# Optimization experiments

Measured on AMD Instinct MI355X. Metric: run time of the kernel, lower is better.

Reference implementation:

```python
import jax, jax.numpy as jnp
import numpy as np

DIM = 512
N_HEADS = 8
N_KV_HEADS = 4
HEAD_DIM = DIM // N_HEADS  # 64
N_REP = N_HEADS // N_KV_HEADS  # 2
THETA = 10000.0
EPS_RMS = 1e-6
EPS_Z = 1e-6


def setup_inputs() -> dict:
    key = jax.random.key(0)
    ks = jax.random.split(key, 6)
    s = 1.0 / np.sqrt(DIM)
    return {
        "x": jax.random.normal(ks[0], (4, 8192, DIM), dtype=jnp.float32),
        "norm_w": jnp.ones((DIM,), dtype=jnp.float32),
        "wq": jax.random.normal(ks[1], (DIM, DIM), dtype=jnp.float32) * s,
        "wk": jax.random.normal(ks[2], (N_KV_HEADS * HEAD_DIM, DIM), dtype=jnp.float32) * s,
        "wv": jax.random.normal(ks[3], (N_KV_HEADS * HEAD_DIM, DIM), dtype=jnp.float32) * s,
        "wo": jax.random.normal(ks[4], (DIM, DIM), dtype=jnp.float32) * s,
    }


def _rope_cos_sin(seq_len, head_dim):
    # freqs_cis = polar(1, t * theta^(-2i/d))
    inv = 1.0 / (THETA ** (jnp.arange(0, head_dim, 2, dtype=jnp.float32) / head_dim))
    ang = jnp.arange(seq_len, dtype=jnp.float32)[:, None] * inv[None, :]  # (S, d/2)
    return jnp.cos(ang), jnp.sin(ang)


def _apply_rope(t, cos, sin):
    # t: (B, S, H, d); complex rotation on consecutive pairs
    B, S, H, d = t.shape
    tr = t.reshape(B, S, H, d // 2, 2)
    xr, xi = tr[..., 0], tr[..., 1]
    c = cos[None, :, None, :]  # (1, S, 1, d/2)
    s = sin[None, :, None, :]
    out = jnp.stack([xr * c - xi * s, xr * s + xi * c], axis=-1)
    return out.reshape(B, S, H, d)


def _forward(x, norm_w, wq, wk, wv, wo):
    B, S, _ = x.shape
    # RMSNorm
    x = x * jax.lax.rsqrt(jnp.mean(x * x, axis=-1, keepdims=True) + EPS_RMS) * norm_w
    xq = (x @ wq.T).reshape(B, S, N_HEADS, HEAD_DIM)
    xk = (x @ wk.T).reshape(B, S, N_KV_HEADS, HEAD_DIM)
    xv = (x @ wv.T).reshape(B, S, N_KV_HEADS, HEAD_DIM)
    cos, sin = _rope_cos_sin(S, HEAD_DIM)
    xq = _apply_rope(xq, cos, sin)
    xk = _apply_rope(xk, cos, sin)
    # repeat_kv: (B,S,Hkv,d) -> (B,S,Hkv*n_rep,d)
    keys = jnp.repeat(xk, N_REP, axis=2)
    values = jnp.repeat(xv, N_REP, axis=2)
    # to (B, H, S, d)
    Q = jnp.transpose(xq, (0, 2, 1, 3))
    K = jnp.transpose(keys, (0, 2, 1, 3))
    V = jnp.transpose(values, (0, 2, 1, 3))
    phi = lambda t: jax.nn.elu(t) + 1.0
    Q_lin, K_lin = phi(Q), phi(K)
    # Faithful to source: elementwise product reduced over s -> (B,H,d)
    KV = jnp.einsum('bhsd,bhsd->bhd', K_lin, V)
    K_sum = K_lin.sum(axis=2)  # (B,H,d)
    Z = jnp.einsum('bhsd,bhd->bhs', Q_lin, K_sum)[..., None]  # (B,H,S,1)
    Y = Q_lin * KV[:, :, None, :] / (Z + EPS_Z)  # (B,H,S,d)
    Y = jnp.transpose(Y, (0, 2, 1, 3)).reshape(B, S, N_HEADS * HEAD_DIM)
    return Y @ wo.T


def reference(x, norm_w, wq, wk, wv, wo):
    return _forward(x, norm_w, wq, wk, wv, wo)
```

## Files before the change

### kernel.cpp

```cpp
#include <hip/hip_runtime.h>
#include <cmath>

typedef __attribute__((ext_vector_type(8))) short short8;
typedef __attribute__((ext_vector_type(4))) float floatx4;

#define T_TOK 32768
#define DIMK 512

__device__ __forceinline__ unsigned short f2bf(float f) {
  union { float f; unsigned int u; } v; v.f = f;
  unsigned int r = (v.u + 0x7fffu + ((v.u >> 16) & 1u)) >> 16;
  return (unsigned short)r;
}
__device__ __forceinline__ float bf2f(unsigned short h) {
  union { unsigned int u; float f; } v; v.u = ((unsigned int)h) << 16;
  return v.f;
}

__device__ __forceinline__ void gload_lds16(const unsigned short* g, unsigned short* ldsbase) {
  __builtin_amdgcn_global_load_lds(
      (const __attribute__((address_space(1))) unsigned int*)g,
      (__attribute__((address_space(3))) unsigned int*)ldsbase, 16, 0, 0);
}

__global__ __launch_bounds__(256) void k_prep(const float* __restrict__ x,
    const float* __restrict__ norm_w, const float* __restrict__ wq,
    const float* __restrict__ wk, const float* __restrict__ wv,
    const float* __restrict__ wo, unsigned short* __restrict__ Wb,
    unsigned short* __restrict__ wob, float2* __restrict__ rope,
    float* __restrict__ KVz, unsigned short* __restrict__ xn) {
  if (blockIdx.x < 2048) {
    int i = blockIdx.x * 256 + threadIdx.x;
    float v;
    if (i < 262144) {
      v = wq[i];
    } else {
      int R = i >> 9, col = i & 511;
      int h = (R - 512) >> 7, rem = (R - 512) & 127;
      if (rem < 64) v = wk[(h * 64 + rem) * 512 + col];
      else          v = wv[(h * 64 + rem - 64) * 512 + col];
    }
    Wb[i] = f2bf(v);
    if (i < 262144) {
      wob[i] = f2bf(wo[i]);
      int s = i >> 5, m = i & 31;
      const double c0 = 0.74989420933245582;
      double c1 = c0 * c0, c2 = c1 * c1, c3 = c2 * c2, c4 = c3 * c3;
      double p = 1.0;
      if (m & 1)  p *= c0;
      if (m & 2)  p *= c1;
      if (m & 4)  p *= c2;
      if (m & 8)  p *= c3;
      if (m & 16) p *= c4;
      double ang = (double)s * p;
      const double TWO_PI = 6.2831853071795864769;
      double q = rint(ang * (1.0 / TWO_PI));
      double r = fma(-q, TWO_PI, ang);
      float rf = (float)r;
      rope[i] = make_float2(cosf(rf), sinf(rf));
    }
    if (i < 2048) KVz[i] = 0.f;
  } else {
    int bid = blockIdx.x - 2048;
    int wave = threadIdx.x >> 6, lane = threadIdx.x & 63;
    size_t t = (size_t)bid * 4 + wave;
    const float4* xr = (const float4*)(x + t * DIMK);
    float4 a = xr[lane * 2];
    float4 b = xr[lane * 2 + 1];
    float ss = a.x * a.x + a.y * a.y + a.z * a.z + a.w * a.w
             + b.x * b.x + b.y * b.y + b.z * b.z + b.w * b.w;
    #pragma unroll
    for (int off = 32; off >= 1; off >>= 1) ss += __shfl_xor(ss, off, 64);
    float scale = rsqrtf(ss * (1.0f / DIMK) + 1e-6f);
    const float4* wr = (const float4*)norm_w;
    float4 w0 = wr[lane * 2], w1 = wr[lane * 2 + 1];
    uint4 o;
    o.x = (unsigned int)f2bf(a.x * scale * w0.x) | ((unsigned int)f2bf(a.y * scale * w0.y) << 16);
    o.y = (unsigned int)f2bf(a.z * scale * w0.z) | ((unsigned int)f2bf(a.w * scale * w0.w) << 16);
    o.z = (unsigned int)f2bf(b.x * scale * w1.x) | ((unsigned int)f2bf(b.y * scale * w1.y) << 16);
    o.w = (unsigned int)f2bf(b.z * scale * w1.z) | ((unsigned int)f2bf(b.w * scale * w1.w) << 16);
    *(uint4*)(xn + t * DIMK + lane * 8) = o;
  }
}

template <bool BF16_OUT, bool FUSE>
__global__ __launch_bounds__(512, 2) void k_gemm256(const unsigned short* __restrict__ A,
    const unsigned short* __restrict__ Bw, void* __restrict__ Cv, int ldc,
    const float2* __restrict__ rope, float* __restrict__ KV, float* __restrict__ Ksum) {
  constexpr int K = DIMK;
  extern __shared__ __align__(16) unsigned short smem[];
  unsigned short* const AsP = smem;
  unsigned short* const BsP = smem + 32768;

  const int tid = threadIdx.x;
  const int wave = tid >> 6, lane = tid & 63;
  const int r = lane & 15, quad = lane >> 4, r7 = r & 7;
  const int wm = (wave >> 2) * 128, wn = (wave & 3) * 64;

  const int ngy = gridDim.y;
  const int bid = blockIdx.x + gridDim.x * blockIdx.y;
  const int xcd = bid & 7;
  const int j = bid >> 3;
  const int lg = (ngy == 4) ? 2 : 1;
  const int per = (gridDim.x * ngy) >> (3 + lg);
  const int mt = xcd * per + (j >> lg);
  const int nt = j & (ngy - 1);
  const int m0 = mt * 256, n0 = nt * 256;

  const int srow = lane >> 3;
  const int scb = (lane & 7) ^ srow;
  const unsigned short* const Asrc = A + (size_t)(m0 + wave * 8 + srow) * K + scb * 8;
  const unsigned short* const Bsrc = Bw + (size_t)(n0 + wave * 8 + srow) * K + scb * 8;
  unsigned short* const Adst = AsP + wave * 8 * 64;
  unsigned short* const Bdst = BsP + wave * 8 * 64;

#define STAGE_A(buf, h, kt) do { \
    gload_lds16(Asrc + (size_t)((h) * 128) * K + (kt) * 64, Adst + (buf) * 16384 + ((h) * 128) * 64); \
    gload_lds16(Asrc + (size_t)((h) * 128 + 64) * K + (kt) * 64, Adst + (buf) * 16384 + ((h) * 128 + 64) * 64); \
  } while (0)
#define STAGE_B(buf, h, kt) do { \
    gload_lds16(Bsrc + (size_t)((h) * 128) * K + (kt) * 64, Bdst + (buf) * 16384 + ((h) * 128) * 64); \
    gload_lds16(Bsrc + (size_t)((h) * 128 + 64) * K + (kt) * 64, Bdst + (buf) * 16384 + ((h) * 128 + 64) * 64); \
  } while (0)

  short8 af[4][2], b0[2][2], b1[2][2];
  floatx4 acc[8][4];
  #pragma unroll
  for (int i = 0; i < 8; i++)
    #pragma unroll
    for (int jj = 0; jj < 4; jj++)
      acc[i][jj] = (floatx4){0.f, 0.f, 0.f, 0.f};

#define LDA8(buf, ah) do { \
    _Pragma("unroll") for (int ii = 0; ii < 4; ii++) \
      _Pragma("unroll") for (int kk = 0; kk < 2; kk++) \
        af[ii][kk] = *(const short8*)&AsP[(buf) * 16384 + (wm + (ah) * 64 + ii * 16 + r) * 64 + ((kk * 4 + quad) ^ r7) * 8]; \
  } while (0)
#define LDB4(buf, bh, arr) do { \
    _Pragma("unroll") for (int jj = 0; jj < 2; jj++) \
      _Pragma("unroll") for (int kk = 0; kk < 2; kk++) \
        arr[jj][kk] = *(const short8*)&BsP[(buf) * 16384 + (wn + (bh) * 32 + jj * 16 + r) * 64 + ((kk * 4 + quad) ^ r7) * 8]; \
  } while (0)
#define MFMAQ(ah, bh, arr) do { \
    __builtin_amdgcn_s_setprio(1); \
    _Pragma("unroll") for (int ii = 0; ii < 4; ii++) \
      _Pragma("unroll") for (int jj = 0; jj < 2; jj++) \
        _Pragma("unroll") for (int kk = 0; kk < 2; kk++) \
          acc[(ah) * 4 + ii][(bh) * 2 + jj] = __builtin_amdgcn_mfma_f32_16x16x32_bf16( \
              af[ii][kk], arr[jj][kk], acc[(ah) * 4 + ii][(bh) * 2 + jj], 0, 0, 0); \
    __builtin_amdgcn_s_setprio(0); \
  } while (0)
#define BAR() do { asm volatile("" ::: "memory"); __builtin_amdgcn_s_barrier(); asm volatile("" ::: "memory"); } while (0)
#define VMW(n) do { asm volatile("s_waitcnt vmcnt(" #n ")" ::: "memory"); __builtin_amdgcn_sched_barrier(0); } while (0)

  STAGE_A(0, 0, 0); STAGE_B(0, 0, 0); STAGE_A(0, 1, 0); STAGE_B(0, 1, 0);
  STAGE_A(1, 0, 1); STAGE_B(1, 0, 1); STAGE_A(1, 1, 1); STAGE_B(1, 1, 1);
  VMW(8);
  BAR();

  #pragma unroll
  for (int it = 0; it < 3; ++it) {
    const int kt = it * 2;
    LDA8(0, 0); LDB4(0, 0, b0);
    BAR(); MFMAQ(0, 0, b0); BAR();
    LDB4(0, 1, b1);
    BAR(); MFMAQ(0, 1, b1); BAR();
    LDA8(0, 1); STAGE_B(0, 0, kt + 2); STAGE_B(0, 1, kt + 2);
    BAR(); MFMAQ(1, 1, b1); BAR();
    STAGE_A(0, 0, kt + 2); STAGE_A(0, 1, kt + 2);
    BAR(); MFMAQ(1, 0, b0); VMW(8); BAR();
    LDA8(1, 0); LDB4(1, 0, b0);
    BAR(); MFMAQ(0, 0, b0); BAR();
    LDB4(1, 1, b1);
    BAR(); MFMAQ(0, 1, b1); BAR();
    LDA8(1, 1); STAGE_B(1, 0, kt + 3); STAGE_B(1, 1, kt + 3);
    BAR(); MFMAQ(1, 1, b1); BAR();
    STAGE_A(1, 0, kt + 3); STAGE_A(1, 1, kt + 3);
    BAR(); MFMAQ(1, 0, b0); VMW(8); BAR();
  }

  LDA8(0, 0); LDB4(0, 0, b0);
  BAR(); MFMAQ(0, 0, b0); BAR();
  LDB4(0, 1, b1);
  BAR(); MFMAQ(0, 1, b1); BAR();
  LDA8(0, 1);
  BAR(); MFMAQ(1, 1, b1); BAR();
  MFMAQ(1, 0, b0); VMW(0); BAR();
  LDA8(1, 0); LDB4(1, 0, b0);
  BAR(); MFMAQ(0, 0, b0); BAR();
  LDB4(1, 1, b1);
  BAR(); MFMAQ(0, 1, b1); BAR();
  LDA8(1, 1);
  BAR(); MFMAQ(1, 1, b1); BAR();
  MFMAQ(1, 0, b0);

  if (FUSE && n0 >= 512) {
    const int b = m0 >> 13;
    const int kh = ((n0 - 512) >> 8) * 2 + (wn >> 7);
    const int hvb = (wn >> 7) << 6;
    float* const Vs = (float*)smem;
    __syncthreads();
    if (wn & 64) {
      #pragma unroll
      for (int i = 0; i < 8; i++)
        #pragma unroll
        for (int j2 = 0; j2 < 4; j2++)
          #pragma unroll
          for (int p = 0; p < 4; p++) {
            int t = wm + i * 16 + quad * 4 + p;
            Vs[t * 128 + hvb + j2 * 16 + r] = acc[i][j2][p];
          }
    }
    __syncthreads();
    if (!(wn & 64)) {
      float kvp[4] = {0.f, 0.f, 0.f, 0.f};
      float ksp[4] = {0.f, 0.f, 0.f, 0.f};
      #pragma unroll
      for (int i = 0; i < 8; i++)
        #pragma unroll
        for (int p = 0; p < 4; p++) {
          int t = wm + i * 16 + quad * 4 + p;
          int pos = (m0 + t) & 8191;
          #pragma unroll
          for (int j2 = 0; j2 < 4; j2++) {
            float v = acc[i][j2][p];
            float vp = __shfl_xor(v, 1, 64);
            int d = j2 * 16 + r;
            float2 cs = rope[pos * 32 + (d >> 1)];
            float rk = (r & 1) ? (vp * cs.y + v * cs.x) : (v * cs.x - vp * cs.y);
            rk = rk > 0.f ? rk + 1.f : __expf(rk);
            kvp[j2] += rk * Vs[t * 128 + hvb + d];
            ksp[j2] += rk;
          }
        }
      #pragma unroll
      for (int j2 = 0; j2 < 4; j2++) {
        kvp[j2] += __shfl_xor(kvp[j2], 16, 64); kvp[j2] += __shfl_xor(kvp[j2], 32, 64);
        ksp[j2] += __shfl_xor(ksp[j2], 16, 64); ksp[j2] += __shfl_xor(ksp[j2], 32, 64);
      }
      if (lane < 16) {
        int base = (b * 4 + kh) * 64 + r;
        #pragma unroll
        for (int j2 = 0; j2 < 4; j2++) {
          atomicAdd(&KV[base + j2 * 16], kvp[j2]);
          atomicAdd(&Ksum[base + j2 * 16], ksp[j2]);
        }
      }
    }
  } else {
    #pragma unroll
    for (int i = 0; i < 8; i++)
      #pragma unroll
      for (int j2 = 0; j2 < 4; j2++) {
        int row = m0 + wm + i * 16 + quad * 4;
        int col = n0 + wn + j2 * 16 + r;
        #pragma unroll
        for (int p = 0; p < 4; p++) {
          if constexpr (BF16_OUT) {
            ((unsigned short*)Cv)[(size_t)(row + p) * ldc + col] = f2bf(acc[i][j2][p]);
          } else {
            ((float*)Cv)[(size_t)(row + p) * ldc + col] = acc[i][j2][p];
          }
        }
      }
  }
#undef STAGE_A
#undef STAGE_B
#undef LDA8
#undef LDB4
#undef MFMAQ
#undef BAR
#undef VMW
}

__global__ __launch_bounds__(256) void k_qkern(const unsigned short* __restrict__ qkv,
    const float2* __restrict__ rope, const float* __restrict__ KV,
    const float* __restrict__ Ksum, unsigned short* __restrict__ Yb) {
  const int h = threadIdx.x >> 5;
  const int pr = threadIdx.x & 31;
  for (int t = blockIdx.x; t < T_TOK; t += gridDim.x) {
    int b = t >> 13, pos = t & 8191;
    unsigned int qp = *(const unsigned int*)(qkv + (size_t)t * 512 + h * 64 + 2 * pr);
    float qx = bf2f((unsigned short)(qp & 0xffffu));
    float qy = bf2f((unsigned short)(qp >> 16));
    float2 cs = rope[pos * 32 + pr];
    float ar = qx * cs.x - qy * cs.y;
    float ai = qx * cs.y + qy * cs.x;
    ar = ar > 0.f ? ar + 1.f : __expf(ar);
    ai = ai > 0.f ? ai + 1.f : __expf(ai);
    int bk = b * 4 + (h >> 1);
    float2 ks = *(const float2*)(Ksum + bk * 64 + 2 * pr);
    float z = ar * ks.x + ai * ks.y;
    #pragma unroll
    for (int off = 16; off >= 1; off >>= 1) z += __shfl_xor(z, off, 64);
    float2 kv = *(const float2*)(KV + bk * 64 + 2 * pr);
    float inv = 1.0f / (z + 1e-6f);
    unsigned int o = (unsigned int)f2bf(ar * kv.x * inv)
                   | ((unsigned int)f2bf(ai * kv.y * inv) << 16);
    *(unsigned int*)(Yb + (size_t)t * 512 + h * 64 + 2 * pr) = o;
  }
}

extern "C" void kernel_launch(void* const* d_in, const int* in_sizes, int n_in,
                              void* d_out, int out_size, void* d_ws, size_t ws_size,
                              hipStream_t stream) {
  const float* x = (const float*)d_in[0];
  const float* norm_w = (const float*)d_in[1];
  const float* wq = (const float*)d_in[2];
  const float* wk = (const float*)d_in[3];
  const float* wv = (const float*)d_in[4];
  const float* wo = (const float*)d_in[5];
  float* out = (float*)d_out;

  char* ws = (char*)d_ws;
  unsigned short* xn  = (unsigned short*)(ws);
  unsigned short* Wb  = (unsigned short*)(ws + 33554432);
  unsigned short* wob = (unsigned short*)(ws + 34603008);
  unsigned short* qkv = (unsigned short*)(ws + 35127296);
  float2* rope        = (float2*)(ws + 102236160);
  float* KV           = (float*)(ws + 104333312);
  float* Ksum         = (float*)(ws + 104337408);
  unsigned short* Yb  = (unsigned short*)(ws + 104341504);

  static bool s_attr = false;
  if (!s_attr) {
    (void)hipFuncSetAttribute(reinterpret_cast<const void*>(&k_gemm256<true, true>),
                              hipFuncAttributeMaxDynamicSharedMemorySize, 131072);
    (void)hipFuncSetAttribute(reinterpret_cast<const void*>(&k_gemm256<false, false>),
                              hipFuncAttributeMaxDynamicSharedMemorySize, 131072);
    s_attr = true;
  }

  k_prep<<<10240, 256, 0, stream>>>(x, norm_w, wq, wk, wv, wo, Wb, wob, rope, KV, xn);
  k_gemm256<true, true><<<dim3(128, 4), 512, 131072, stream>>>(
      xn, Wb, (void*)qkv, 512, rope, KV, Ksum);
  k_qkern<<<4096, 256, 0, stream>>>(qkv, rope, KV, Ksum, Yb);
  k_gemm256<false, false><<<dim3(128, 2), 512, 131072, stream>>>(
      Yb, wob, (void*)out, 512, nullptr, nullptr, nullptr);
}
```

Baseline: 220.3 us.

## Store GEMM operands in K-panel-major layout and swizzle the V staging buffer

```diff
diff --git a/kernel.cpp b/kernel.cpp
--- a/kernel.cpp
+++ b/kernel.cpp
@@ -6,6 +6,7 @@
 
 #define T_TOK 32768
 #define DIMK 512
+#define AKT 2097152
 
 __device__ __forceinline__ unsigned short f2bf(float f) {
   union { float f; unsigned int u; } v; v.f = f;
@@ -31,18 +32,18 @@
     float* __restrict__ KVz, unsigned short* __restrict__ xn) {
   if (blockIdx.x < 2048) {
     int i = blockIdx.x * 256 + threadIdx.x;
+    int R = i >> 9, col = i & 511;
     float v;
     if (i < 262144) {
       v = wq[i];
     } else {
-      int R = i >> 9, col = i & 511;
       int h = (R - 512) >> 7, rem = (R - 512) & 127;
       if (rem < 64) v = wk[(h * 64 + rem) * 512 + col];
       else          v = wv[(h * 64 + rem - 64) * 512 + col];
     }
-    Wb[i] = f2bf(v);
+    Wb[(col >> 6) * 65536 + R * 64 + (col & 63)] = f2bf(v);
     if (i < 262144) {
-      wob[i] = f2bf(wo[i]);
+      wob[(col >> 6) * 32768 + R * 64 + (col & 63)] = f2bf(wo[i]);
       int s = i >> 5, m = i & 31;
       const double c0 = 0.74989420933245582;
       double c1 = c0 * c0, c2 = c1 * c1, c3 = c2 * c2, c4 = c3 * c3;
@@ -79,15 +80,14 @@
     o.y = (unsigned int)f2bf(a.z * scale * w0.z) | ((unsigned int)f2bf(a.w * scale * w0.w) << 16);
     o.z = (unsigned int)f2bf(b.x * scale * w1.x) | ((unsigned int)f2bf(b.y * scale * w1.y) << 16);
     o.w = (unsigned int)f2bf(b.z * scale * w1.z) | ((unsigned int)f2bf(b.w * scale * w1.w) << 16);
-    *(uint4*)(xn + t * DIMK + lane * 8) = o;
+    *(uint4*)(xn + (size_t)(lane >> 3) * AKT + t * 64 + (lane & 7) * 8) = o;
   }
 }
 
 template <bool BF16_OUT, bool FUSE>
 __global__ __launch_bounds__(512, 2) void k_gemm256(const unsigned short* __restrict__ A,
-    const unsigned short* __restrict__ Bw, void* __restrict__ Cv, int ldc,
+    const unsigned short* __restrict__ Bw, void* __restrict__ Cv, int ldc, int nrows,
     const float2* __restrict__ rope, float* __restrict__ KV, float* __restrict__ Ksum) {
-  constexpr int K = DIMK;
   extern __shared__ __align__(16) unsigned short smem[];
   unsigned short* const AsP = smem;
   unsigned short* const BsP = smem + 32768;
@@ -109,18 +109,19 @@
 
   const int srow = lane >> 3;
   const int scb = (lane & 7) ^ srow;
-  const unsigned short* const Asrc = A + (size_t)(m0 + wave * 8 + srow) * K + scb * 8;
-  const unsigned short* const Bsrc = Bw + (size_t)(n0 + wave * 8 + srow) * K + scb * 8;
+  const size_t bkt = (size_t)nrows * 64;
+  const unsigned short* const Asrc = A + (size_t)(m0 + wave * 8 + srow) * 64 + scb * 8;
+  const unsigned short* const Bsrc = Bw + (size_t)(n0 + wave * 8 + srow) * 64 + scb * 8;
   unsigned short* const Adst = AsP + wave * 8 * 64;
   unsigned short* const Bdst = BsP + wave * 8 * 64;
 
 #define STAGE_A(buf, h, kt) do { \
-    gload_lds16(Asrc + (size_t)((h) * 128) * K + (kt) * 64, Adst + (buf) * 16384 + ((h) * 128) * 64); \
-    gload_lds16(Asrc + (size_t)((h) * 128 + 64) * K + (kt) * 64, Adst + (buf) * 16384 + ((h) * 128 + 64) * 64); \
+    gload_lds16(Asrc + (size_t)(kt) * AKT + (h) * 8192, Adst + (buf) * 16384 + ((h) * 128) * 64); \
+    gload_lds16(Asrc + (size_t)(kt) * AKT + (h) * 8192 + 4096, Adst + (buf) * 16384 + ((h) * 128 + 64) * 64); \
   } while (0)
 #define STAGE_B(buf, h, kt) do { \
-    gload_lds16(Bsrc + (size_t)((h) * 128) * K + (kt) * 64, Bdst + (buf) * 16384 + ((h) * 128) * 64); \
-    gload_lds16(Bsrc + (size_t)((h) * 128 + 64) * K + (kt) * 64, Bdst + (buf) * 16384 + ((h) * 128 + 64) * 64); \
+    gload_lds16(Bsrc + (size_t)(kt) * bkt + (h) * 8192, Bdst + (buf) * 16384 + ((h) * 128) * 64); \
+    gload_lds16(Bsrc + (size_t)(kt) * bkt + (h) * 8192 + 4096, Bdst + (buf) * 16384 + ((h) * 128 + 64) * 64); \
   } while (0)
 
   short8 af[4][2], b0[2][2], b1[2][2];
@@ -195,6 +196,7 @@
   MFMAQ(1, 0, b0);
 
   if (FUSE && n0 >= 512) {
+#define VSW(t, d) ((t) * 128 + ((d) & 15) + (((((d) >> 4) + ((t) >> 2)) & 7) << 4))
     const int b = m0 >> 13;
     const int kh = ((n0 - 512) >> 8) * 2 + (wn >> 7);
     const int hvb = (wn >> 7) << 6;
@@ -208,7 +210,7 @@
           #pragma unroll
           for (int p = 0; p < 4; p++) {
             int t = wm + i * 16 + quad * 4 + p;
-            Vs[t * 128 + hvb + j2 * 16 + r] = acc[i][j2][p];
+            Vs[VSW(t, hvb + j2 * 16 + r)] = acc[i][j2][p];
           }
     }
     __syncthreads();
@@ -229,7 +231,7 @@
             float2 cs = rope[pos * 32 + (d >> 1)];
             float rk = (r & 1) ? (vp * cs.y + v * cs.x) : (v * cs.x - vp * cs.y);
             rk = rk > 0.f ? rk + 1.f : __expf(rk);
-            kvp[j2] += rk * Vs[t * 128 + hvb + d];
+            kvp[j2] += rk * Vs[VSW(t, hvb + d)];
             ksp[j2] += rk;
           }
         }
@@ -247,6 +249,7 @@
         }
       }
     }
+#undef VSW
   } else {
     #pragma unroll
     for (int i = 0; i < 8; i++)
@@ -297,7 +300,7 @@
     float inv = 1.0f / (z + 1e-6f);
     unsigned int o = (unsigned int)f2bf(ar * kv.x * inv)
                    | ((unsigned int)f2bf(ai * kv.y * inv) << 16);
-    *(unsigned int*)(Yb + (size_t)t * 512 + h * 64 + 2 * pr) = o;
+    *(unsigned int*)(Yb + (size_t)h * AKT + t * 64 + 2 * pr) = o;
   }
 }
 
@@ -333,8 +336,8 @@
 
   k_prep<<<10240, 256, 0, stream>>>(x, norm_w, wq, wk, wv, wo, Wb, wob, rope, KV, xn);
   k_gemm256<true, true><<<dim3(128, 4), 512, 131072, stream>>>(
-      xn, Wb, (void*)qkv, 512, rope, KV, Ksum);
+      xn, Wb, (void*)qkv, 512, 1024, rope, KV, Ksum);
   k_qkern<<<4096, 256, 0, stream>>>(qkv, rope, KV, Ksum, Yb);
   k_gemm256<false, false><<<dim3(128, 2), 512, 131072, stream>>>(
-      Yb, wob, (void*)out, 512, nullptr, nullptr, nullptr);
-}
+      Yb, wob, (void*)out, 512, 512, nullptr, nullptr, nullptr);
+}
```

Result: no change. 219.3 us (-0.5%).
